# Kernel tuning notes

Measured on AMD Instinct MI355X. Metric: run time of the kernel, lower is better.

Reference implementation:

```python
import jax, jax.numpy as jnp
import numpy as np

EMBED_DIM = 1024
NUM_HEADS = 16
HEAD_DIM = EMBED_DIM // NUM_HEADS


def setup_inputs() -> dict:
    key = jax.random.key(0)
    ks = jax.random.split(key, 5)
    scale = 1.0 / np.sqrt(EMBED_DIM)
    x = jax.random.normal(ks[0], (2, 2048, EMBED_DIM), dtype=jnp.float32)
    W_qkv = jax.random.uniform(ks[1], (EMBED_DIM, 3 * EMBED_DIM), jnp.float32, -scale, scale)
    b_qkv = jax.random.uniform(ks[2], (3 * EMBED_DIM,), jnp.float32, -scale, scale)
    W_out = jax.random.uniform(ks[3], (EMBED_DIM, EMBED_DIM), jnp.float32, -scale, scale)
    b_out = jax.random.uniform(ks[4], (EMBED_DIM,), jnp.float32, -scale, scale)
    return {"x": x, "W_qkv": W_qkv, "b_qkv": b_qkv, "W_out": W_out, "b_out": b_out}


def reference(x, W_qkv, b_qkv, W_out, b_out):
    B, T, C = x.shape
    H, D = NUM_HEADS, HEAD_DIM
    qkv = x @ W_qkv + b_qkv                       # [B,T,3C]
    q, k, v = jnp.split(qkv, 3, axis=-1)
    # [B,T,C] -> [B,H,T,D]
    q = q.reshape(B, T, H, D).transpose(0, 2, 1, 3)
    k = k.reshape(B, T, H, D).transpose(0, 2, 1, 3)
    v = v.reshape(B, T, H, D).transpose(0, 2, 1, 3)
    scores = jnp.einsum('bhqd,bhkd->bhqk', q, k) / np.sqrt(D)
    attn = jax.nn.softmax(scores, axis=-1)
    out = jnp.einsum('bhqk,bhkd->bhqd', attn, v)  # [B,H,T,D]
    out = out.transpose(0, 2, 1, 3).reshape(B, T, C)
    return out @ W_out + b_out
```

## Files before the change

### kernel.cpp

```cpp
#include <hip/hip_runtime.h>
#include <hip/hip_bf16.h>

#define TB 2048
#define CC 1024
#define HH 16
#define DD 64
#define MM 4096
#define N3 3072
#define KVB 128
#define NT (TB / KVB)

typedef __bf16 bf16x8 __attribute__((ext_vector_type(8)));
typedef float f32x4 __attribute__((ext_vector_type(4)));
typedef float f32x16 __attribute__((ext_vector_type(16)));
typedef unsigned short ushort8 __attribute__((ext_vector_type(8)));
typedef unsigned short u16;

#define QSCALE 0.180336880693612f

__device__ __forceinline__ u16 f2b(float f) {
    unsigned int x = __float_as_uint(f);
    x = (x + 0x7fffu + ((x >> 16) & 1u)) >> 16;
    return (u16)x;
}

__device__ __forceinline__ unsigned cvt_pk_bf16(float lo, float hi) {
    unsigned r;
    asm("v_cvt_pk_bf16_f32 %0, %1, %2" : "=v"(r) : "v"(lo), "v"(hi));
    return r;
}

__device__ __forceinline__ void gld16(const u16* g, u16* l) {
    __builtin_amdgcn_global_load_lds(
        (const __attribute__((address_space(1))) unsigned int*)g,
        (__attribute__((address_space(3))) unsigned int*)l, 16, 0, 0);
}

__global__ __launch_bounds__(256) void prep(const float* __restrict__ x,
                                            u16* __restrict__ xb,
                                            const float* __restrict__ wqkv,
                                            u16* __restrict__ wqkvT,
                                            const float* __restrict__ wout,
                                            u16* __restrict__ woutT) {
    __shared__ float tl[64][65];
    const int bx = blockIdx.x;
    const int tid = threadIdx.x;
    if (bx < 4096) {
        int i = (bx * 256 + tid) * 4;
        float4 v = *reinterpret_cast<const float4*>(x + i);
        union { u16 u[4]; uint2 v2; } r;
        r.u[0] = f2b(v.x); r.u[1] = f2b(v.y); r.u[2] = f2b(v.z); r.u[3] = f2b(v.w);
        *reinterpret_cast<uint2*>(xb + i) = r.v2;
        return;
    }
    const int idx = bx - 4096;
    const int nb = idx & 63, kb = idx >> 6;
    const float* in; u16* out; int N, n0;
    if (nb < 48) { in = wqkv; out = wqkvT; N = 3072; n0 = nb * 64; }
    else         { in = wout; out = woutT; N = 1024; n0 = (nb - 48) * 64; }
    const int k0 = kb * 64;
#pragma unroll
    for (int rep = 0; rep < 16; ++rep) {
        int id2 = rep * 256 + tid;
        int r = id2 >> 6, c = id2 & 63;
        tl[r][c] = in[(size_t)(k0 + r) * N + n0 + c];
    }
    __syncthreads();
#pragma unroll
    for (int rep = 0; rep < 16; ++rep) {
        int id2 = rep * 256 + tid;
        int r = id2 >> 6, c = id2 & 63;
        out[(size_t)(n0 + r) * 1024 + k0 + c] = f2b(tl[c][r]);
    }
}

__global__ __launch_bounds__(512, 2) void gemm_qkv(const u16* __restrict__ xb,
                                                   const u16* __restrict__ wT,
                                                   const float* __restrict__ bias,
                                                   u16* __restrict__ qg,
                                                   u16* __restrict__ kg,
                                                   u16* __restrict__ vtg) {
    __shared__ u16 smem[65536];
    u16* const A0 = smem;
    u16* const B0 = smem + 16384;
    u16* const A1 = smem + 32768;
    u16* const B1 = smem + 49152;
    const int id = blockIdx.y * 12 + blockIdx.x;
    const int xcd = id & 7, pos = id >> 3;
    const int m0 = ((xcd >> 1) * 4 + pos / 6) * 256;
    const int n0 = ((xcd & 1) * 6 + pos % 6) * 256;
    const int tid = threadIdx.x;
    const int w = tid >> 6, lane = tid & 63, lr = lane & 15, h = lane >> 4;
    const int wr = w >> 2, wc = w & 3;
    f32x4 acc[8][4] = {};
    bf16x8 bB[4][2];
    bf16x8 a[2][2];

#define STAGE_SIDE(dstb, srcp, rowbase, kt) do {                                      \
    _Pragma("unroll")                                                                 \
    for (int jj = 0; jj < 4; ++jj) {                                                  \
        int L = jj * 512 + tid;                                                       \
        int rr = L >> 3, c8 = L & 7;                                                  \
        gld16((srcp) + (size_t)((rowbase) + rr) * 1024 + (kt) * 64                    \
                  + ((c8 ^ (rr & 7)) << 3),                                           \
              (dstb) + L * 8);                                                        \
    } } while (0)
#define DSREAD_B(PB) do {                                                             \
    _Pragma("unroll")                                                                 \
    for (int n = 0; n < 4; ++n) {                                                     \
        int R = wc * 64 + n * 16 + lr;                                                \
        const char* br = (const char*)(PB) + R * 128;                                 \
        bB[n][0] = *reinterpret_cast<const bf16x8*>(br + ((h ^ (R & 7)) << 4));       \
        bB[n][1] = *reinterpret_cast<const bf16x8*>(br + (((4 + h) ^ (R & 7)) << 4)); \
    } } while (0)
#define DSREAD_A(PA, mb) do {                                                         \
    _Pragma("unroll")                                                                 \
    for (int mi = 0; mi < 2; ++mi) {                                                  \
        int R = wr * 128 + ((mb) + mi) * 16 + lr;                                     \
        const char* ar = (const char*)(PA) + R * 128;                                 \
        a[mi][0] = *reinterpret_cast<const bf16x8*>(ar + ((h ^ (R & 7)) << 4));       \
        a[mi][1] = *reinterpret_cast<const bf16x8*>(ar + (((4 + h) ^ (R & 7)) << 4)); \
    } } while (0)
#define MFMAP(mb) do {                                                                \
    _Pragma("unroll")                                                                 \
    for (int mi = 0; mi < 2; ++mi)                                                    \
        _Pragma("unroll")                                                             \
        for (int n = 0; n < 4; ++n) {                                                 \
            acc[(mb) + mi][n] = __builtin_amdgcn_mfma_f32_16x16x32_bf16(              \
                a[mi][0], bB[n][0], acc[(mb) + mi][n], 0, 0, 0);                      \
            acc[(mb) + mi][n] = __builtin_amdgcn_mfma_f32_16x16x32_bf16(              \
                a[mi][1], bB[n][1], acc[(mb) + mi][n], 0, 0, 0);                      \
        } } while (0)
#define GBAR __builtin_amdgcn_s_barrier()
#define VMC(n) asm volatile("s_waitcnt vmcnt(" #n ")" ::: "memory")
#define LGK0 do { asm volatile("s_waitcnt lgkmcnt(0)" ::: "memory");                  \
                  __builtin_amdgcn_sched_barrier(0); } while (0)
#define PRI1 __builtin_amdgcn_s_setprio(1)
#define PRI0 __builtin_amdgcn_s_setprio(0)

    STAGE_SIDE(A0, xb, m0, 0);
    STAGE_SIDE(B0, wT, n0, 0);

#pragma unroll 1
    for (int i = 0; i < 7; ++i) {
        const int t1 = 2 * i + 1, t2 = 2 * i + 2;
        STAGE_SIDE(A1, xb, m0, t1);
        VMC(4); GBAR;
        DSREAD_B(B0); DSREAD_A(A0, 0); LGK0;
        PRI1; MFMAP(0); PRI0; GBAR;
        STAGE_SIDE(B1, wT, n0, t1);
        DSREAD_A(A0, 2); GBAR; LGK0; PRI1; MFMAP(2); PRI0; GBAR;
        DSREAD_A(A0, 4); GBAR; LGK0; PRI1; MFMAP(4); PRI0; GBAR;
        DSREAD_A(A0, 6); GBAR; LGK0; PRI1; MFMAP(6); PRI0; GBAR;
        STAGE_SIDE(A0, xb, m0, t2);
        VMC(4); GBAR;
        DSREAD_B(B1); DSREAD_A(A1, 0); LGK0;
        PRI1; MFMAP(0); PRI0; GBAR;
        STAGE_SIDE(B0, wT, n0, t2);
        DSREAD_A(A1, 2); GBAR; LGK0; PRI1; MFMAP(2); PRI0; GBAR;
        DSREAD_A(A1, 4); GBAR; LGK0; PRI1; MFMAP(4); PRI0; GBAR;
        DSREAD_A(A1, 6); GBAR; LGK0; PRI1; MFMAP(6); PRI0; GBAR;
    }
    STAGE_SIDE(A1, xb, m0, 15);
    VMC(4); GBAR;
    DSREAD_B(B0); DSREAD_A(A0, 0); LGK0;
    PRI1; MFMAP(0); PRI0; GBAR;
    STAGE_SIDE(B1, wT, n0, 15);
    DSREAD_A(A0, 2); GBAR; LGK0; PRI1; MFMAP(2); PRI0; GBAR;
    DSREAD_A(A0, 4); GBAR; LGK0; PRI1; MFMAP(4); PRI0; GBAR;
    DSREAD_A(A0, 6); GBAR; LGK0; PRI1; MFMAP(6); PRI0; GBAR;
    VMC(0); GBAR;
    DSREAD_B(B1); DSREAD_A(A1, 0); LGK0;
    PRI1; MFMAP(0); PRI0; GBAR;
    DSREAD_A(A1, 2); GBAR; LGK0; PRI1; MFMAP(2); PRI0; GBAR;
    DSREAD_A(A1, 4); GBAR; LGK0; PRI1; MFMAP(4); PRI0; GBAR;
    DSREAD_A(A1, 6); GBAR; LGK0; PRI1; MFMAP(6); PRI0; GBAR;

#undef STAGE_SIDE
#undef DSREAD_B
#undef DSREAD_A
#undef MFMAP
#undef GBAR
#undef VMC
#undef LGK0
#undef PRI1
#undef PRI0

    const int nthird = n0 >> 10;
    const int b = m0 >> 11, t0 = m0 & 2047;
    float bv[4];
#pragma unroll
    for (int n = 0; n < 4; ++n)
        bv[n] = bias[n0 + wc * 64 + n * 16 + lr];

    __syncthreads();
    if (nthird == 2) {
#pragma unroll
        for (int n = 0; n < 4; ++n) {
            int nloc = wc * 64 + n * 16 + lr;
#pragma unroll
            for (int m = 0; m < 8; ++m) {
                int mloc = wr * 128 + m * 16 + h * 4;
                int mpb = (mloc & ~15) | ((mloc & 4) << 1) | ((mloc & 8) >> 1);
                union { u16 u[4]; unsigned long long ll; } pk4;
#pragma unroll
                for (int reg = 0; reg < 4; ++reg)
                    pk4.u[reg] = f2b(acc[m][n][reg] + bv[n]);
                int slot = mpb >> 3;
                *reinterpret_cast<unsigned long long*>(
                    (char*)smem + nloc * 512 + (((slot ^ (nloc & 31)) << 4) | ((mpb & 7) * 2))) = pk4.ll;
            }
        }
        __syncthreads();
#pragma unroll
        for (int pass = 0; pass < 16; ++pass) {
            int cid = pass * 512 + tid;
            int r = cid >> 5, p = cid & 31;
            ushort8 vch = *reinterpret_cast<const ushort8*>((const char*)smem + r * 512 + (p << 4));
            int tb = p ^ (r & 31);
            int c1 = (n0 & 1023) + r;
            int hh = c1 >> 6, dd = c1 & 63;
            *reinterpret_cast<ushort8*>(
                vtg + ((size_t)(b * HH + hh) * DD + dd) * TB + t0 + tb * 8) = vch;
        }
    } else {
        const float qs = (nthird == 0) ? QSCALE : 1.0f;
#pragma unroll
        for (int m = 0; m < 8; ++m) {
            int rb = wr * 128 + m * 16 + h * 4;
#pragma unroll
            for (int n = 0; n < 4; ++n) {
                int c = wc * 64 + n * 16 + lr;
#pragma unroll
                for (int reg = 0; reg < 4; ++reg) {
                    int r = rb + reg;
                    *reinterpret_cast<u16*>((char*)smem + r * 512 +
                        ((((c >> 3) ^ (r & 31)) << 4) | ((c & 7) << 1)))
                        = f2b((acc[m][n][reg] + bv[n]) * qs);
                }
            }
        }
        __syncthreads();
        u16* dst = (nthird == 0) ? qg : kg;
#pragma unroll
        for (int pass = 0; pass < 16; ++pass) {
            int cid = pass * 512 + tid;
            int r = cid >> 5, p = cid & 31;
            ushort8 vch = *reinterpret_cast<const ushort8*>((const char*)smem + r * 512 + (p << 4));
            int cb = p ^ (r & 31);
            int c1 = (n0 & 1023) + cb * 8;
            int hh = c1 >> 6, dd = c1 & 63;
            *reinterpret_cast<ushort8*>(
                dst + ((size_t)(b * HH + hh) * TB + t0 + r) * DD + dd) = vch;
        }
    }
}

__global__ __launch_bounds__(256, 2) void attn(const u16* __restrict__ qg,
                                               const u16* __restrict__ kg,
                                               const u16* __restrict__ vtg,
                                               u16* __restrict__ ao) {
    __shared__ u16 Kt[2][KVB * 64];
    __shared__ u16 Vt[2][64 * KVB];
    const int bh = blockIdx.x;
    const int q0 = blockIdx.y * 128;
    const int tid = threadIdx.x, w = tid >> 6, lane = tid & 63;
    const int ln = lane & 31, H = lane >> 5;
    const u16* qb = qg + (size_t)bh * TB * DD;
    const u16* kb = kg + (size_t)bh * TB * DD;
    const u16* vb = vtg + (size_t)bh * DD * TB;

#define STAGE(buf, kp, vp) do {                                                         \
    _Pragma("unroll")                                                                   \
    for (int j = 0; j < 4; ++j) {                                                       \
        int L = j * 256 + tid;                                                          \
        int rk = L >> 3, ck = L & 7;                                                    \
        gld16((kp) + (size_t)rk * DD + ((ck ^ (rk & 7)) << 3), Kt[buf] + L * 8);        \
        int rv = L >> 4, cv = L & 15;                                                   \
        gld16((vp) + (size_t)rv * TB + ((cv ^ (rv & 15)) << 3), Vt[buf] + L * 8);       \
    } } while (0)

    bf16x8 bq[4];
#pragma unroll
    for (int dc = 0; dc < 4; ++dc)
        bq[dc] = *reinterpret_cast<const bf16x8*>(
            qb + (size_t)(q0 + w * 32 + ln) * DD + dc * 16 + H * 8);

    f32x16 o[2] = {};
    float m_r = -1e30f;
    float l_r = 0.f;
    f32x16 zero16 = {};

    auto tile_body = [&](const u16* ktc, const u16* vtc) {
        f32x16 s[4];
        __builtin_amdgcn_s_setprio(1);
#pragma unroll
        for (int kb4 = 0; kb4 < 4; ++kb4) {
            int R = kb4 * 32 + ln;
            const char* krow = (const char*)ktc + R * 128;
#pragma unroll
            for (int dc = 0; dc < 4; ++dc) {
                bf16x8 ak = *reinterpret_cast<const bf16x8*>(
                    krow + (((dc * 2 + H) ^ (R & 7)) << 4));
                s[kb4] = __builtin_amdgcn_mfma_f32_32x32x16_bf16(
                    ak, bq[dc], dc == 0 ? zero16 : s[kb4], 0, 0, 0);
            }
        }
        __builtin_amdgcn_s_setprio(0);

        float pm = s[0][0];
#pragma unroll
        for (int kb4 = 0; kb4 < 4; ++kb4) {
            float t0 = fmaxf(fmaxf(s[kb4][0], s[kb4][1]), fmaxf(s[kb4][2], s[kb4][3]));
            float t1 = fmaxf(fmaxf(s[kb4][4], s[kb4][5]), fmaxf(s[kb4][6], s[kb4][7]));
            float t2 = fmaxf(fmaxf(s[kb4][8], s[kb4][9]), fmaxf(s[kb4][10], s[kb4][11]));
            float t3 = fmaxf(fmaxf(s[kb4][12], s[kb4][13]), fmaxf(s[kb4][14], s[kb4][15]));
            pm = fmaxf(pm, fmaxf(fmaxf(t0, t1), fmaxf(t2, t3)));
        }
        pm = fmaxf(pm, __shfl_xor(pm, 32));

        if (!__all(pm - m_r <= 8.0f)) {
            float mn = fmaxf(m_r, pm);
            float fr = __builtin_amdgcn_exp2f(m_r - mn);
            m_r = mn;
            l_r *= fr;
#pragma unroll
            for (int ngd = 0; ngd < 2; ++ngd)
#pragma unroll
                for (int r = 0; r < 16; ++r)
                    o[ngd][r] *= fr;
        }

        float sum = 0.f;
#pragma unroll
        for (int kb4 = 0; kb4 < 4; ++kb4) {
            float ps = 0.f;
#pragma unroll
            for (int r = 0; r < 16; ++r) {
                s[kb4][r] = __builtin_amdgcn_exp2f(s[kb4][r] - m_r);
                ps += s[kb4][r];
            }
            sum += ps;
        }
        sum += __shfl_xor(sum, 32);
        l_r += sum;

        __builtin_amdgcn_s_setprio(1);
#pragma unroll
        for (int kb4 = 0; kb4 < 4; ++kb4) {
#pragma unroll
            for (int b1 = 0; b1 < 2; ++b1) {
                union { unsigned u[4]; bf16x8 v; } ap;
                ap.u[0] = cvt_pk_bf16(s[kb4][8 * b1 + 0], s[kb4][8 * b1 + 1]);
                ap.u[1] = cvt_pk_bf16(s[kb4][8 * b1 + 2], s[kb4][8 * b1 + 3]);
                ap.u[2] = cvt_pk_bf16(s[kb4][8 * b1 + 4], s[kb4][8 * b1 + 5]);
                ap.u[3] = cvt_pk_bf16(s[kb4][8 * b1 + 6], s[kb4][8 * b1 + 7]);
                int c = kb4 * 2 + b1;
#pragma unroll
                for (int ngd = 0; ngd < 2; ++ngd) {
                    int d = ngd * 32 + ln;
                    bf16x8 av = *reinterpret_cast<const bf16x8*>(
                        (const char*)vtc + d * 256 + (((c * 2 + H) ^ (d & 15)) << 4));
                    o[ngd] = __builtin_amdgcn_mfma_f32_32x32x16_bf16(av, ap.v, o[ngd], 0, 0, 0);
                }
            }
        }
        __builtin_amdgcn_s_setprio(0);
    };

    STAGE(0, kb, vb);
    const u16* kp = kb + KVB * DD;
    const u16* vp = vb + KVB;
    __syncthreads();

#pragma unroll 1
    for (int kt2 = 0; kt2 < NT / 2; ++kt2) {
        STAGE(1, kp, vp);
        kp += KVB * DD; vp += KVB;
        tile_body(Kt[0], Vt[0]);
        __syncthreads();
        if (kt2 < NT / 2 - 1) {
            STAGE(0, kp, vp);
            kp += KVB * DD; vp += KVB;
        }
        tile_body(Kt[1], Vt[1]);
        __syncthreads();
    }
#undef STAGE

    const float linv = 1.0f / l_r;
    const int b = bh >> 4, hh = bh & 15;
    const int q = q0 + w * 32 + ln;
    u16* aorow = ao + (size_t)(b * TB + q) * CC + hh * 64;
#pragma unroll
    for (int ngd = 0; ngd < 2; ++ngd) {
#pragma unroll
        for (int rg = 0; rg < 4; ++rg) {
            int dbase = ngd * 32 + 8 * rg + 4 * H;
            union { u16 u[4]; unsigned long long ll; } pk;
#pragma unroll
            for (int r2 = 0; r2 < 4; ++r2)
                pk.u[r2] = f2b(o[ngd][4 * rg + r2] * linv);
            *reinterpret_cast<unsigned long long*>(aorow + dbase) = pk.ll;
        }
    }
}

__global__ __launch_bounds__(256) void gemm_out(const u16* __restrict__ ao,
                                                const u16* __restrict__ wT,
                                                const float* __restrict__ bias,
                                                float* __restrict__ out) {
    __shared__ u16 As[64 * 64];
    __shared__ u16 Bs[128 * 64];
    const int id = blockIdx.y * 8 + blockIdx.x;
    const int xcd = id & 7, pos = id >> 3;
    const int xr = xcd >> 1, xc = xcd & 1;
    const int pr = pos >> 2, pc = pos & 3;
    const int m0 = (xr * 16 + pr) * 64;
    const int n0 = (xc * 4 + pc) * 128;
    const int tid = threadIdx.x;
    const int w = tid >> 6, lane = tid & 63, lr = lane & 15, h = lane >> 4;
    f32x4 acc[4][2] = {};

    for (int k0 = 0; k0 < 1024; k0 += 64) {
        __syncthreads();
#pragma unroll
        for (int j = 0; j < 2; ++j) {
            int L = j * 256 + tid;
            int r = L >> 3, c = L & 7;
            gld16(ao + (size_t)(m0 + r) * 1024 + k0 + ((c ^ (r & 7)) << 3), As + L * 8);
        }
#pragma unroll
        for (int j = 0; j < 4; ++j) {
            int L = j * 256 + tid;
            int r = L >> 3, c = L & 7;
            gld16(wT + (size_t)(n0 + r) * 1024 + k0 + ((c ^ (r & 7)) << 3), Bs + L * 8);
        }
        __syncthreads();
#pragma unroll
        for (int kk = 0; kk < 2; ++kk) {
            bf16x8 a[4], b[2];
            int cc = kk * 4 + h;
#pragma unroll
            for (int m = 0; m < 4; ++m) {
                int R = m * 16 + lr;
                a[m] = *reinterpret_cast<const bf16x8*>((const char*)As + R * 128 + ((cc ^ (R & 7)) << 4));
            }
#pragma unroll
            for (int n = 0; n < 2; ++n) {
                int R = w * 32 + n * 16 + lr;
                b[n] = *reinterpret_cast<const bf16x8*>((const char*)Bs + R * 128 + ((cc ^ (R & 7)) << 4));
            }
#pragma unroll
            for (int m = 0; m < 4; ++m)
#pragma unroll
                for (int n = 0; n < 2; ++n)
                    acc[m][n] = __builtin_amdgcn_mfma_f32_16x16x32_bf16(a[m], b[n], acc[m][n], 0, 0, 0);
        }
    }

#pragma unroll
    for (int n = 0; n < 2; ++n) {
        int ng = n0 + w * 32 + n * 16 + lr;
        float bv = bias[ng];
#pragma unroll
        for (int m = 0; m < 4; ++m) {
#pragma unroll
            for (int reg = 0; reg < 4; ++reg) {
                int mg = m0 + m * 16 + h * 4 + reg;
                out[(size_t)mg * 1024 + ng] = acc[m][n][reg] + bv;
            }
        }
    }
}

extern "C" void kernel_launch(void* const* d_in, const int* in_sizes, int n_in,
                              void* d_out, int out_size, void* d_ws, size_t ws_size,
                              hipStream_t stream) {
    const float* x     = (const float*)d_in[0];
    const float* W_qkv = (const float*)d_in[1];
    const float* b_qkv = (const float*)d_in[2];
    const float* W_out = (const float*)d_in[3];
    const float* b_out = (const float*)d_in[4];
    float* out = (float*)d_out;

    char* ws = (char*)d_ws;
    u16* xb    = (u16*)(ws);
    u16* wqkvT = (u16*)(ws + (size_t)( 8u << 20));
    u16* woutT = (u16*)(ws + (size_t)(14u << 20));
    u16* qg    = (u16*)(ws + (size_t)(16u << 20));
    u16* kg    = (u16*)(ws + (size_t)(24u << 20));
    u16* vtg   = (u16*)(ws + (size_t)(32u << 20));
    u16* ao    = xb;

    hipLaunchKernelGGL(prep, dim3(5120), dim3(256), 0, stream, x, xb, W_qkv, wqkvT, W_out, woutT);
    hipLaunchKernelGGL(gemm_qkv, dim3(12, 16), dim3(512), 0, stream, xb, wqkvT, b_qkv, qg, kg, vtg);
    hipLaunchKernelGGL(attn, dim3(32, 16), dim3(256), 0, stream, qg, kg, vtg, ao);
    hipLaunchKernelGGL(gemm_out, dim3(8, 64), dim3(256), 0, stream, ao, woutT, b_out, out);
}
```

Measured before the change: 110.1 us.

## Double-buffer out-projection GEMM loads and vectorize weight transpose accesses

The output-projection GEMM now uses two LDS buffers, prefetching the next K tile with async global-to-LDS loads while MFMAs run on the current one, synchronised with explicit vmcnt waits and barriers. The MFMA section is also raised in wave priority. Separately, the weight transpose/convert kernel now reads float4 and writes packed 4-element bf16 stores instead of scalar accesses. The prefetch doubles LDS use for the GEMM and depends on hand-counted waitcnt values being correct.

```diff
diff --git a/kernel.cpp b/kernel.cpp
--- a/kernel.cpp
+++ b/kernel.cpp
@@ -60,17 +60,22 @@
     else         { in = wout; out = woutT; N = 1024; n0 = (nb - 48) * 64; }
     const int k0 = kb * 64;
 #pragma unroll
-    for (int rep = 0; rep < 16; ++rep) {
-        int id2 = rep * 256 + tid;
-        int r = id2 >> 6, c = id2 & 63;
-        tl[r][c] = in[(size_t)(k0 + r) * N + n0 + c];
+    for (int rep = 0; rep < 4; ++rep) {
+        int r = rep * 16 + (tid >> 4);
+        int c4 = (tid & 15) * 4;
+        float4 v = *reinterpret_cast<const float4*>(&in[(size_t)(k0 + r) * N + n0 + c4]);
+        tl[r][c4] = v.x; tl[r][c4 + 1] = v.y; tl[r][c4 + 2] = v.z; tl[r][c4 + 3] = v.w;
     }
     __syncthreads();
 #pragma unroll
-    for (int rep = 0; rep < 16; ++rep) {
-        int id2 = rep * 256 + tid;
-        int r = id2 >> 6, c = id2 & 63;
-        out[(size_t)(n0 + r) * 1024 + k0 + c] = f2b(tl[c][r]);
+    for (int rep = 0; rep < 4; ++rep) {
+        int nn = rep * 16 + (tid >> 4);
+        int kk4 = (tid & 15) * 4;
+        union { u16 u[4]; unsigned long long ll; } pk;
+#pragma unroll
+        for (int i = 0; i < 4; ++i)
+            pk.u[i] = f2b(tl[kk4 + i][nn]);
+        *reinterpret_cast<unsigned long long*>(&out[(size_t)(n0 + nn) * 1024 + k0 + kk4]) = pk.ll;
     }
 }
 
@@ -410,8 +415,8 @@
                                                 const u16* __restrict__ wT,
                                                 const float* __restrict__ bias,
                                                 float* __restrict__ out) {
-    __shared__ u16 As[64 * 64];
-    __shared__ u16 Bs[128 * 64];
+    __shared__ u16 As[2][64 * 64];
+    __shared__ u16 Bs[2][128 * 64];
     const int id = blockIdx.y * 8 + blockIdx.x;
     const int xcd = id & 7, pos = id >> 3;
     const int xr = xcd >> 1, xc = xcd & 1;
@@ -422,21 +427,33 @@
     const int w = tid >> 6, lane = tid & 63, lr = lane & 15, h = lane >> 4;
     f32x4 acc[4][2] = {};
 
-    for (int k0 = 0; k0 < 1024; k0 += 64) {
-        __syncthreads();
-#pragma unroll
-        for (int j = 0; j < 2; ++j) {
-            int L = j * 256 + tid;
-            int r = L >> 3, c = L & 7;
-            gld16(ao + (size_t)(m0 + r) * 1024 + k0 + ((c ^ (r & 7)) << 3), As + L * 8);
-        }
-#pragma unroll
-        for (int j = 0; j < 4; ++j) {
-            int L = j * 256 + tid;
-            int r = L >> 3, c = L & 7;
-            gld16(wT + (size_t)(n0 + r) * 1024 + k0 + ((c ^ (r & 7)) << 3), Bs + L * 8);
-        }
-        __syncthreads();
+#define GO_STAGE(buf, kt) do {                                                        \
+    _Pragma("unroll")                                                                 \
+    for (int j = 0; j < 2; ++j) {                                                     \
+        int L = j * 256 + tid;                                                        \
+        int r = L >> 3, c = L & 7;                                                    \
+        gld16(ao + (size_t)(m0 + r) * 1024 + (kt) * 64 + ((c ^ (r & 7)) << 3),        \
+              As[buf] + L * 8);                                                       \
+    }                                                                                 \
+    _Pragma("unroll")                                                                 \
+    for (int j = 0; j < 4; ++j) {                                                     \
+        int L = j * 256 + tid;                                                        \
+        int r = L >> 3, c = L & 7;                                                    \
+        gld16(wT + (size_t)(n0 + r) * 1024 + (kt) * 64 + ((c ^ (r & 7)) << 3),        \
+              Bs[buf] + L * 8);                                                       \
+    } } while (0)
+
+    GO_STAGE(0, 0);
+    int cur = 0;
+#pragma unroll 1
+    for (int kt = 0; kt < 16; ++kt) {
+        if (kt < 15) {
+            GO_STAGE(cur ^ 1, kt + 1);
+            asm volatile("s_waitcnt vmcnt(6)" ::: "memory");
+        } else {
+            asm volatile("s_waitcnt vmcnt(0)" ::: "memory");
+        }
+        __builtin_amdgcn_s_barrier();
 #pragma unroll
         for (int kk = 0; kk < 2; ++kk) {
             bf16x8 a[4], b[2];
@@ -444,20 +461,26 @@
 #pragma unroll
             for (int m = 0; m < 4; ++m) {
                 int R = m * 16 + lr;
-                a[m] = *reinterpret_cast<const bf16x8*>((const char*)As + R * 128 + ((cc ^ (R & 7)) << 4));
+                a[m] = *reinterpret_cast<const bf16x8*>((const char*)As[cur] + R * 128 + ((cc ^ (R & 7)) << 4));
             }
 #pragma unroll
             for (int n = 0; n < 2; ++n) {
                 int R = w * 32 + n * 16 + lr;
-                b[n] = *reinterpret_cast<const bf16x8*>((const char*)Bs + R * 128 + ((cc ^ (R & 7)) << 4));
-            }
+                b[n] = *reinterpret_cast<const bf16x8*>((const char*)Bs[cur] + R * 128 + ((cc ^ (R & 7)) << 4));
+            }
+            __builtin_amdgcn_s_setprio(1);
 #pragma unroll
             for (int m = 0; m < 4; ++m)
 #pragma unroll
                 for (int n = 0; n < 2; ++n)
                     acc[m][n] = __builtin_amdgcn_mfma_f32_16x16x32_bf16(a[m], b[n], acc[m][n], 0, 0, 0);
-        }
-    }
+            __builtin_amdgcn_s_setprio(0);
+        }
+        __builtin_amdgcn_sched_barrier(0);
+        __builtin_amdgcn_s_barrier();
+        cur ^= 1;
+    }
+#undef GO_STAGE
 
 #pragma unroll
     for (int n = 0; n < 2; ++n) {
```

Result: no change. 110.3 us (median of 2 runs) (+0.2%).
